# Kernel tuning notes

Hardware: AMD Instinct MI355X
Metric: run time of the kernel (lower is better)

The kernel has to match this reference:

```python
import jax, jax.numpy as jnp
import numpy as np

HEAD_DIM = 128
PROJ_DIM = 64


def setup_inputs() -> dict:
    key = jax.random.key(0)
    kq, kk, kv, kr = jax.random.split(key, 4)
    B, H, NQ, NKV = 1, 16, 2048, 4096
    Q = jax.random.normal(kq, (B, H, NQ, HEAD_DIM), dtype=jnp.float32)
    K = jax.random.normal(kk, (B, H, NKV, HEAD_DIM), dtype=jnp.float32)
    V = jax.random.normal(kv, (B, H, NKV, HEAD_DIM), dtype=jnp.float32)
    # R ~ N(0,1) / sqrt(proj_dim), as in the torch __init__
    R = jax.random.normal(kr, (HEAD_DIM, PROJ_DIM), dtype=jnp.float32) / (PROJ_DIM ** 0.5)
    return {"Q": Q, "K": K, "V": V, "R": R}


def reference(Q, K, V, R):
    proj_dim = R.shape[-1]
    scale = 1.0 / (proj_dim ** 0.5)
    # Project Q and K into the random-projection space: [B,H,N,proj_dim]
    Q_proj = jnp.einsum('bhnd,dp->bhnp', Q, R)
    K_proj = jnp.einsum('bhmd,dp->bhmp', K, R)
    # scores: [B,H,NQ,NKV]
    scores = jnp.einsum('bhnp,bhmp->bhnm', Q_proj, K_proj) * scale
    weights = jax.nn.softmax(scores, axis=-1)
    # output: [B,H,NQ,head_dim]
    return jnp.einsum('bhnm,bhmd->bhnd', weights, V)
```

## Files before the change

kernel.cpp:

```cpp
#include <hip/hip_runtime.h>

#define HEADS 16
#define NQ    2048
#define NKV   4096
#define DH    128
#define PDIM  64

typedef __bf16 bf16_t;
typedef bf16_t bf16x8 __attribute__((ext_vector_type(8)));
typedef bf16_t bf16x4 __attribute__((ext_vector_type(4)));
typedef bf16_t bf16x2 __attribute__((ext_vector_type(2)));
typedef float  f32x4  __attribute__((ext_vector_type(4)));
typedef float  f32x16 __attribute__((ext_vector_type(16)));
typedef int    i32x4  __attribute__((ext_vector_type(4)));

typedef __attribute__((address_space(3))) unsigned int       lds_u32;
typedef __attribute__((address_space(1))) const unsigned int glb_u32;

__device__ __forceinline__ void dma16(const void* g, void* l) {
  __builtin_amdgcn_global_load_lds((glb_u32*)g, (lds_u32*)l, 16, 0, 0);
}

__global__ __launch_bounds__(256) void prep_kernel(
    const float* __restrict__ Q, const float* __restrict__ K,
    const float* __restrict__ V, const float* __restrict__ R,
    bf16_t* __restrict__ Qp, bf16_t* __restrict__ Kp, bf16_t* __restrict__ Vt)
{
  __shared__ float  sF[64 * 132];
  __shared__ bf16_t sY[4][16 * 72];
  const int tid = threadIdx.x;
  const int bid = blockIdx.x;

  const int isQ = (bid < 512);
  const int isK = (bid >= 512) && (bid < 1536);

  const float* src;
  long row0;
  if (isQ)      { src = Q; row0 = (long)bid * 64; }
  else if (isK) { src = K; row0 = (long)(bid - 512) * 64; }
  else          { src = V; row0 = (long)(bid - 1536) * 64; }
  const float* tp = src + row0 * DH;
#pragma unroll
  for (int rep = 0; rep < 8; ++rep) {
    const int slot = tid + rep * 256;
    const int j = slot >> 5, c4 = (slot & 31) * 4;
    f32x4 v = *(const f32x4*)(tp + j * DH + c4);
    *(f32x4*)(&sF[j * 132 + c4]) = v;
  }
  __syncthreads();

  if (!isQ && !isK) {
    const int vb = bid - 1536;
    const int h = vb >> 6, jt = vb & 63;
    bf16_t* op = Vt + (long)h * DH * NKV + jt * 64;
#pragma unroll
    for (int rep = 0; rep < 4; ++rep) {
      const int slot = tid + rep * 256;
      const int d = slot >> 3, j8 = (slot & 7) * 8;
      bf16x8 w;
#pragma unroll
      for (int jj = 0; jj < 8; ++jj) w[jj] = (bf16_t)sF[(j8 + jj) * 132 + d];
      *(bf16x8*)(op + (long)d * NKV + j8) = w;
    }
    return;
  }

  const int wave = tid >> 6, lane = tid & 63;
  const int n16  = lane & 15, quad = lane >> 4;
  const float scale = isQ ? 0.18033688011112042f : 1.0f;
  bf16_t* Y = isQ ? Qp : Kp;

  bf16x8 bfr[4][4];
#pragma unroll
  for (int nt = 0; nt < 4; ++nt) {
    const int n = nt * 16 + n16;
#pragma unroll
    for (int kk = 0; kk < 4; ++kk) {
      const int k0 = kk * 32 + quad * 8;
      bf16x8 b;
#pragma unroll
      for (int j = 0; j < 8; ++j) b[j] = (bf16_t)R[(k0 + j) * PDIM + n];
      bfr[nt][kk] = b;
    }
  }

  const int arow = wave * 16 + n16;
  bf16x8 a[4];
#pragma unroll
  for (int kk = 0; kk < 4; ++kk) {
    const int k0 = kk * 32 + quad * 8;
    f32x4 x0 = *(const f32x4*)(&sF[arow * 132 + k0]);
    f32x4 x1 = *(const f32x4*)(&sF[arow * 132 + k0 + 4]);
    bf16x8 av;
#pragma unroll
    for (int j = 0; j < 4; ++j) { av[j] = (bf16_t)(x0[j] * scale); av[4 + j] = (bf16_t)(x1[j] * scale); }
    a[kk] = av;
  }

  bf16_t* sy = sY[wave];
#pragma unroll
  for (int nt = 0; nt < 4; ++nt) {
    f32x4 acc = {0.f, 0.f, 0.f, 0.f};
#pragma unroll
    for (int kk = 0; kk < 4; ++kk)
      acc = __builtin_amdgcn_mfma_f32_16x16x32_bf16(a[kk], bfr[nt][kk], acc, 0, 0, 0);
#pragma unroll
    for (int r = 0; r < 4; ++r)
      sy[(quad * 4 + r) * 72 + nt * 16 + n16] = (bf16_t)acc[r];
  }
  const long xrow = row0 + wave * 16;
  const int row = lane >> 2, cg = lane & 3;
  bf16x8 w0 = *(const bf16x8*)(&sy[row * 72 + cg * 16]);
  bf16x8 w1 = *(const bf16x8*)(&sy[row * 72 + cg * 16 + 8]);
  *(bf16x8*)(Y + (xrow + row) * PDIM + cg * 16)     = w0;
  *(bf16x8*)(Y + (xrow + row) * PDIM + cg * 16 + 8) = w1;
}

__global__ __launch_bounds__(128, 2) void flash_kernel(
    const bf16_t* __restrict__ Qp, const bf16_t* __restrict__ Kp,
    const bf16_t* __restrict__ Vt, bf16_t* __restrict__ Opart,
    float* __restrict__ Lpart, float* __restrict__ Out,
    int splits, int iters)
{
  __shared__ char smem[24576];
  bf16_t* sK = (bf16_t*)smem;
  bf16_t* sV = (bf16_t*)(smem + 8192);

  const int tid  = threadIdx.x;
  const int wave = tid >> 6, lane = tid & 63;
  const int l31  = lane & 31, h = lane >> 5;

  const int head = blockIdx.x & 15;
  const int qt   = (blockIdx.x >> 4) & 15;
  const int sp   = blockIdx.x >> 8;

  const int qbase = qt * 128 + wave * 64;
  const int kv0   = sp * (64 * iters);

  bf16x8 qf[2][4];
#pragma unroll
  for (int qsub = 0; qsub < 2; ++qsub)
#pragma unroll
    for (int k = 0; k < 4; ++k)
      qf[qsub][k] = *(const bf16x8*)(Qp + ((long)head * NQ + qbase + qsub * 32 + l31) * PDIM
                                     + k * 16 + h * 8);

  f32x16 o[2][4] = {};
  float rsum[2] = {0.f, 0.f};

  const bf16_t* kpH = Kp + (long)head * NKV * PDIM;
  const bf16_t* vtH = Vt + (long)head * DH * NKV;

  const int sw = ((lane & 7) ^ ((lane >> 3) & 7)) * 8;
  const int r8 = lane >> 3;

  for (int t = 0; t < iters; ++t) {
    const int kvb = kv0 + t * 64;
    __syncthreads();
    if (wave == 0) {
#pragma unroll
      for (int i = 0; i < 8; ++i)
        dma16(kpH + (long)(kvb + i * 8 + r8) * PDIM + sw, smem + i * 1024);
#pragma unroll
      for (int i = 0; i < 4; ++i)
        dma16(vtH + (long)(i * 8 + r8) * NKV + kvb + sw, smem + 8192 + i * 1024);
    } else {
#pragma unroll
      for (int i = 4; i < 16; ++i)
        dma16(vtH + (long)(i * 8 + r8) * NKV + kvb + sw, smem + 8192 + i * 1024);
    }
    __syncthreads();

#pragma unroll
    for (int s = 0; s < 2; ++s) {
      int bfr[2][2][4];
#pragma unroll
      for (int qsub = 0; qsub < 2; ++qsub) {
        f32x16 sc = {};
        const int r = s * 32 + l31;
#pragma unroll
        for (int k = 0; k < 4; ++k) {
          const int c = 2 * k + h;
          const bf16x8 a = *(const bf16x8*)(sK + r * 64 + ((c ^ (r & 7)) * 8));
          sc = __builtin_amdgcn_mfma_f32_32x32x16_bf16(a, qf[qsub][k], sc, 0, 0, 0);
        }
        int pk[4][2];
#pragma unroll
        for (int rg = 0; rg < 4; ++rg) {
          const float p0 = __builtin_amdgcn_exp2f(sc[rg * 4 + 0]);
          const float p1 = __builtin_amdgcn_exp2f(sc[rg * 4 + 1]);
          const float p2 = __builtin_amdgcn_exp2f(sc[rg * 4 + 2]);
          const float p3 = __builtin_amdgcn_exp2f(sc[rg * 4 + 3]);
          rsum[qsub] += (p0 + p1) + (p2 + p3);
          union { bf16x2 v; int i; } u0, u1;
          u0.v = bf16x2{(bf16_t)p0, (bf16_t)p1};
          u1.v = bf16x2{(bf16_t)p2, (bf16_t)p3};
          pk[rg][0] = u0.i; pk[rg][1] = u1.i;
        }
#pragma unroll
        for (int cl = 0; cl < 2; ++cl) {
          const int e00 = __shfl_xor(pk[2 * cl][0], 32);
          const int e01 = __shfl_xor(pk[2 * cl][1], 32);
          const int e10 = __shfl_xor(pk[2 * cl + 1][0], 32);
          const int e11 = __shfl_xor(pk[2 * cl + 1][1], 32);
          bfr[qsub][cl][0] = h ? e10 : pk[2 * cl][0];
          bfr[qsub][cl][1] = h ? e11 : pk[2 * cl][1];
          bfr[qsub][cl][2] = h ? pk[2 * cl + 1][0] : e00;
          bfr[qsub][cl][3] = h ? pk[2 * cl + 1][1] : e01;
        }
      }
#pragma unroll
      for (int dsub = 0; dsub < 4; ++dsub) {
        const int r = dsub * 32 + l31;
#pragma unroll
        for (int cl = 0; cl < 2; ++cl) {
          const int c = 2 * (2 * s + cl) + h;
          const bf16x8 va = *(const bf16x8*)(sV + r * 64 + ((c ^ (r & 7)) * 8));
#pragma unroll
          for (int qsub = 0; qsub < 2; ++qsub) {
            union { i32x4 i; bf16x8 v; } pb;
            pb.i = i32x4{bfr[qsub][cl][0], bfr[qsub][cl][1],
                         bfr[qsub][cl][2], bfr[qsub][cl][3]};
            o[qsub][dsub] = __builtin_amdgcn_mfma_f32_32x32x16_bf16(va, pb.v, o[qsub][dsub], 0, 0, 0);
          }
        }
      }
    }
  }

  __syncthreads();
  bf16_t* myT = (bf16_t*)(smem + wave * 8704);
#pragma unroll
  for (int qsub = 0; qsub < 2; ++qsub) {
    const float lsum = rsum[qsub] + __shfl_xor(rsum[qsub], 32);
    const float scale = (splits > 1) ? 1.0f : (1.0f / lsum);
#pragma unroll
    for (int dsub = 0; dsub < 4; ++dsub)
#pragma unroll
      for (int rg = 0; rg < 4; ++rg) {
        bf16x4 w = { (bf16_t)(o[qsub][dsub][rg * 4 + 0] * scale),
                     (bf16_t)(o[qsub][dsub][rg * 4 + 1] * scale),
                     (bf16_t)(o[qsub][dsub][rg * 4 + 2] * scale),
                     (bf16_t)(o[qsub][dsub][rg * 4 + 3] * scale) };
        *(bf16x4*)(myT + l31 * 136 + dsub * 32 + rg * 8 + h * 4) = w;
      }
    const int qglob = qbase + qsub * 32;
#pragma unroll
    for (int j = 0; j < 8; ++j) {
      const int ql = j * 4 + (lane >> 4);
      bf16x8 v = *(const bf16x8*)(myT + ql * 136 + (lane & 15) * 8);
      if (splits > 1) {
        *(bf16x8*)(Opart + (((long)sp * HEADS + head) * NQ + qglob + ql) * DH + (lane & 15) * 8) = v;
      } else {
        float* op = Out + ((long)head * NQ + qglob + ql) * DH + (lane & 15) * 8;
        f32x4 a = {(float)v[0], (float)v[1], (float)v[2], (float)v[3]};
        f32x4 b = {(float)v[4], (float)v[5], (float)v[6], (float)v[7]};
        *(f32x4*)op = a; *(f32x4*)(op + 4) = b;
      }
    }
    if (splits > 1 && h == 0)
      Lpart[((long)sp * HEADS + head) * NQ + qglob + l31] = lsum;
  }
}

__global__ __launch_bounds__(256) void combine_kernel(
    const bf16_t* __restrict__ Opart, const float* __restrict__ Lpart,
    float* __restrict__ Out)
{
  const long idx = (long)blockIdx.x * 256 + threadIdx.x;
  const int  d8  = (int)(idx & 15);
  const long hq  = idx >> 4;
  float l = 0.f;
  float acc[8];
#pragma unroll
  for (int j = 0; j < 8; ++j) acc[j] = 0.f;
#pragma unroll
  for (int s = 0; s < 4; ++s) {
    l += Lpart[s * (long)(HEADS * NQ) + hq];
    bf16x8 v = *(const bf16x8*)(Opart + (s * (long)(HEADS * NQ) + hq) * DH + d8 * 8);
#pragma unroll
    for (int j = 0; j < 8; ++j) acc[j] += (float)v[j];
  }
  const float inv = 1.f / l;
  f32x4 o0 = { acc[0] * inv, acc[1] * inv, acc[2] * inv, acc[3] * inv };
  f32x4 o1 = { acc[4] * inv, acc[5] * inv, acc[6] * inv, acc[7] * inv };
  float* op = Out + hq * DH + d8 * 8;
  *(f32x4*)(op)     = o0;
  *(f32x4*)(op + 4) = o1;
}

extern "C" void kernel_launch(void* const* d_in, const int* in_sizes, int n_in,
                              void* d_out, int out_size, void* d_ws, size_t ws_size,
                              hipStream_t stream)
{
  const float* Q = (const float*)d_in[0];
  const float* K = (const float*)d_in[1];
  const float* V = (const float*)d_in[2];
  const float* R = (const float*)d_in[3];
  float* Out = (float*)d_out;

  char* ws = (char*)d_ws;
  bf16_t* Qp = (bf16_t*)(ws);
  bf16_t* Kp = (bf16_t*)(ws + (size_t)(4  << 20));
  bf16_t* Vt = (bf16_t*)(ws + (size_t)(12 << 20));
  bf16_t* Opart = (bf16_t*)(ws + (size_t)(28 << 20));
  float*  Lpart = (float*)(ws + (size_t)(60 << 20));

  const size_t need4 = (size_t)(60 << 20) + 4ull * HEADS * NQ * sizeof(float);
  const int splits = (ws_size >= need4) ? 4 : 1;
  const int iters  = NKV / (64 * splits);

  prep_kernel<<<2560, 256, 0, stream>>>(Q, K, V, R, Qp, Kp, Vt);
  flash_kernel<<<splits * 256, 128, 0, stream>>>(Qp, Kp, Vt, Opart, Lpart, Out,
                                                 splits, iters);
  if (splits == 4)
    combine_kernel<<<2048, 256, 0, stream>>>(Opart, Lpart, Out);
}
```

Measured before the change: 193.9 us.

## Swizzle prep LDS layout, add MFMA priority hints, allow 8-way KV split

```diff
diff --git a/kernel.cpp b/kernel.cpp
--- a/kernel.cpp
+++ b/kernel.cpp
@@ -26,7 +26,7 @@
     const float* __restrict__ V, const float* __restrict__ R,
     bf16_t* __restrict__ Qp, bf16_t* __restrict__ Kp, bf16_t* __restrict__ Vt)
 {
-  __shared__ float  sF[64 * 132];
+  __shared__ float  sF[64 * 128];
   __shared__ bf16_t sY[4][16 * 72];
   const int tid = threadIdx.x;
   const int bid = blockIdx.x;
@@ -43,9 +43,9 @@
 #pragma unroll
   for (int rep = 0; rep < 8; ++rep) {
     const int slot = tid + rep * 256;
-    const int j = slot >> 5, c4 = (slot & 31) * 4;
-    f32x4 v = *(const f32x4*)(tp + j * DH + c4);
-    *(f32x4*)(&sF[j * 132 + c4]) = v;
+    const int j = slot >> 5, g = slot & 31;
+    f32x4 v = *(const f32x4*)(tp + j * DH + g * 4);
+    *(f32x4*)(&sF[j * 128 + ((g ^ ((j >> 3) & 7)) << 2)]) = v;
   }
   __syncthreads();
 
@@ -57,9 +57,11 @@
     for (int rep = 0; rep < 4; ++rep) {
       const int slot = tid + rep * 256;
       const int d = slot >> 3, j8 = (slot & 7) * 8;
+      const int key = slot & 7;
+      const int gsw = (((d >> 2) ^ key) << 2) + (d & 3);
       bf16x8 w;
 #pragma unroll
-      for (int jj = 0; jj < 8; ++jj) w[jj] = (bf16_t)sF[(j8 + jj) * 132 + d];
+      for (int jj = 0; jj < 8; ++jj) w[jj] = (bf16_t)sF[(j8 + jj) * 128 + gsw];
       *(bf16x8*)(op + (long)d * NKV + j8) = w;
     }
     return;
@@ -85,12 +87,14 @@
   }
 
   const int arow = wave * 16 + n16;
+  const int akey = (arow >> 3) & 7;
   bf16x8 a[4];
 #pragma unroll
   for (int kk = 0; kk < 4; ++kk) {
     const int k0 = kk * 32 + quad * 8;
-    f32x4 x0 = *(const f32x4*)(&sF[arow * 132 + k0]);
-    f32x4 x1 = *(const f32x4*)(&sF[arow * 132 + k0 + 4]);
+    const int g0 = k0 >> 2;
+    f32x4 x0 = *(const f32x4*)(&sF[arow * 128 + ((g0 ^ akey) << 2)]);
+    f32x4 x1 = *(const f32x4*)(&sF[arow * 128 + (((g0 + 1) ^ akey) << 2)]);
     bf16x8 av;
 #pragma unroll
     for (int j = 0; j < 4; ++j) { av[j] = (bf16_t)(x0[j] * scale); av[4 + j] = (bf16_t)(x1[j] * scale); }
@@ -178,12 +182,14 @@
       for (int qsub = 0; qsub < 2; ++qsub) {
         f32x16 sc = {};
         const int r = s * 32 + l31;
+        __builtin_amdgcn_s_setprio(1);
 #pragma unroll
         for (int k = 0; k < 4; ++k) {
           const int c = 2 * k + h;
           const bf16x8 a = *(const bf16x8*)(sK + r * 64 + ((c ^ (r & 7)) * 8));
           sc = __builtin_amdgcn_mfma_f32_32x32x16_bf16(a, qf[qsub][k], sc, 0, 0, 0);
         }
+        __builtin_amdgcn_s_setprio(0);
         int pk[4][2];
 #pragma unroll
         for (int rg = 0; rg < 4; ++rg) {
@@ -209,6 +215,7 @@
           bfr[qsub][cl][3] = h ? pk[2 * cl + 1][1] : e01;
         }
       }
+      __builtin_amdgcn_s_setprio(1);
 #pragma unroll
       for (int dsub = 0; dsub < 4; ++dsub) {
         const int r = dsub * 32 + l31;
@@ -225,6 +232,7 @@
           }
         }
       }
+      __builtin_amdgcn_s_setprio(0);
     }
   }
 
@@ -265,7 +273,7 @@
 
 __global__ __launch_bounds__(256) void combine_kernel(
     const bf16_t* __restrict__ Opart, const float* __restrict__ Lpart,
-    float* __restrict__ Out)
+    float* __restrict__ Out, int splits)
 {
   const long idx = (long)blockIdx.x * 256 + threadIdx.x;
   const int  d8  = (int)(idx & 15);
@@ -274,8 +282,7 @@
   float acc[8];
 #pragma unroll
   for (int j = 0; j < 8; ++j) acc[j] = 0.f;
-#pragma unroll
-  for (int s = 0; s < 4; ++s) {
+  for (int s = 0; s < splits; ++s) {
     l += Lpart[s * (long)(HEADS * NQ) + hq];
     bf16x8 v = *(const bf16x8*)(Opart + (s * (long)(HEADS * NQ) + hq) * DH + d8 * 8);
 #pragma unroll
@@ -303,16 +310,21 @@
   bf16_t* Qp = (bf16_t*)(ws);
   bf16_t* Kp = (bf16_t*)(ws + (size_t)(4  << 20));
   bf16_t* Vt = (bf16_t*)(ws + (size_t)(12 << 20));
-  bf16_t* Opart = (bf16_t*)(ws + (size_t)(28 << 20));
-  float*  Lpart = (float*)(ws + (size_t)(60 << 20));
-
-  const size_t need4 = (size_t)(60 << 20) + 4ull * HEADS * NQ * sizeof(float);
-  const int splits = (ws_size >= need4) ? 4 : 1;
-  const int iters  = NKV / (64 * splits);
+
+  const size_t base   = (size_t)28 << 20;
+  const size_t oBytes = (size_t)HEADS * NQ * DH * 2;
+  const size_t lBytes = (size_t)HEADS * NQ * 4;
+  int splits = 1;
+  if (ws_size >= base + 8 * (oBytes + lBytes))      splits = 8;
+  else if (ws_size >= base + 4 * (oBytes + lBytes)) splits = 4;
+
+  bf16_t* Opart = (bf16_t*)(ws + base);
+  float*  Lpart = (float*)(ws + base + (size_t)splits * oBytes);
+  const int iters = NKV / (64 * splits);
 
   prep_kernel<<<2560, 256, 0, stream>>>(Q, K, V, R, Qp, Kp, Vt);
   flash_kernel<<<splits * 256, 128, 0, stream>>>(Qp, Kp, Vt, Opart, Lpart, Out,
                                                  splits, iters);
-  if (splits == 4)
-    combine_kernel<<<2048, 256, 0, stream>>>(Opart, Lpart, Out);
-}
+  if (splits > 1)
+    combine_kernel<<<2048, 256, 0, stream>>>(Opart, Lpart, Out, splits);
+}
```

After: 268.9 us. +38.7%, slower.
